# Kernel optimization log

Hardware: AMD Instinct MI355X
Metric: run time of the kernel (lower is better)

Reference implementation:

```python
import jax, jax.numpy as jnp
import numpy as np

N, M, H, K, CIN, COUT, P = 50000, 50000, 32, 15, 64, 128, 3
KP_EXTENT = 0.072
RADIUS = 0.06


def setup_inputs() -> dict:
    key = jax.random.key(0)
    ks = jax.random.split(key, 7)
    q_pts = jax.random.uniform(ks[0], (N, P), dtype=jnp.float32) * 0.05
    s_pts = jax.random.uniform(ks[1], (M, P), dtype=jnp.float32) * 0.05
    neighb_inds = jax.random.randint(ks[2], (N, H), 0, M, dtype=jnp.int64)
    x = jax.random.normal(ks[3], (M, CIN), dtype=jnp.float32)
    # kernel points inside sphere of radius RADIUS (stand-in for load_kernels)
    kernel_points = jax.random.normal(ks[4], (K, P), dtype=jnp.float32) * (0.5 * RADIUS)
    stddev = np.sqrt(1.0 / (K * COUT)).astype(np.float32)
    weights = jax.random.normal(ks[5], (K, CIN, COUT), dtype=jnp.float32) * stddev
    bias = jnp.zeros((COUT,), dtype=jnp.float32)
    return {"q_pts": q_pts, "s_pts": s_pts, "neighb_inds": neighb_inds,
            "x": x, "kernel_points": kernel_points, "weights": weights, "bias": bias}


def reference(q_pts, s_pts, neighb_inds, x, kernel_points, weights, bias):
    # pad support points with a far-away point and features with a zero row
    s_pad = jnp.concatenate([s_pts, jnp.full((1, s_pts.shape[1]), 1e6, s_pts.dtype)], axis=0)
    x_pad = jnp.concatenate([x, jnp.zeros((1, x.shape[1]), x.dtype)], axis=0)
    # gather neighbor coords/features: [N, H, P], [N, H, CIN]
    neighbors = s_pad[neighb_inds] - q_pts[:, None, :]
    neighb_x = x_pad[neighb_inds]
    # distances to kernel points: [N, H, K]
    diff = neighbors[:, :, None, :] - kernel_points  # [N, H, K, P]
    sq_d = jnp.sum(diff * diff, axis=-1)
    all_weights = jax.nn.relu(1.0 - jnp.sqrt(sq_d) / KP_EXTENT)  # linear influence
    # aggregate: [N, K, CIN] then apply per-kernel-point weights and sum over K
    weighted_features = jnp.einsum('nhk,nhc->nkc', all_weights, neighb_x)
    out = jnp.einsum('nkc,kco->no', weighted_features, weights) + bias  # [N, COUT]
    return out
```

## Files before the change

kernel.cpp:

```cpp
#include <hip/hip_runtime.h>
#include <hip/hip_bf16.h>


#define NPTS   50000
#define NPAD   50048
#define HNB    32
#define KPTS   15
#define CING   64
#define COUTG  128
#define KDIM   960
#define INV_EXT 13.888889f

typedef __attribute__((ext_vector_type(8))) short bf16x8;
typedef __attribute__((ext_vector_type(4))) float f32x4;

static __device__ __forceinline__ unsigned short f2bf(float f) {
    unsigned int u = __float_as_uint(f);
    u += 0x7FFFu + ((u >> 16) & 1u);
    return (unsigned short)(u >> 16);
}

__global__ void kpconv_wt(const float* __restrict__ wgt, unsigned short* __restrict__ Wt) {
    int kc = blockIdx.x;
    int o  = threadIdx.x;
    Wt[(size_t)o * KDIM + kc] = f2bf(wgt[(size_t)kc * COUTG + o]);
}

__global__ __launch_bounds__(256) void kpconv_agg(
    const float* __restrict__ q_pts, const float* __restrict__ s_pts,
    const int* __restrict__ inds, const float* __restrict__ x,
    const float* __restrict__ kpts, unsigned short* __restrict__ wf)
{
    __shared__ float kp[48];
    __shared__ float nb[4][HNB][3];
    __shared__ int   sidx[4][HNB];
    __shared__ float w[4][HNB][16];

    const int tid = threadIdx.x;
    const int g   = tid >> 6;
    const int c   = tid & 63;
    const int n   = blockIdx.x * 4 + g;

    if (tid < 45) kp[tid] = kpts[tid];
    if (c < HNB) {
        int m = inds[n * HNB + c];
        sidx[g][c] = m;
        float qx = q_pts[n * 3 + 0];
        float qy = q_pts[n * 3 + 1];
        float qz = q_pts[n * 3 + 2];
        nb[g][c][0] = s_pts[(size_t)m * 3 + 0] - qx;
        nb[g][c][1] = s_pts[(size_t)m * 3 + 1] - qy;
        nb[g][c][2] = s_pts[(size_t)m * 3 + 2] - qz;
    }
    __syncthreads();

    for (int i = c; i < 512; i += 64) {
        int h = i >> 4, k = i & 15;
        float v = 0.f;
        if (k < KPTS) {
            float dx = nb[g][h][0] - kp[k * 3 + 0];
            float dy = nb[g][h][1] - kp[k * 3 + 1];
            float dz = nb[g][h][2] - kp[k * 3 + 2];
            float d  = sqrtf(dx * dx + dy * dy + dz * dz);
            v = fmaxf(0.f, 1.f - d * INV_EXT);
        }
        w[g][h][k] = v;
    }
    __syncthreads();

    float acc[KPTS];
#pragma unroll
    for (int k = 0; k < KPTS; ++k) acc[k] = 0.f;

#pragma unroll 8
    for (int h = 0; h < HNB; ++h) {
        float xv = x[(size_t)sidx[g][h] * CING + c];
        float4 w0 = *(float4*)&w[g][h][0];
        float4 w1 = *(float4*)&w[g][h][4];
        float4 w2 = *(float4*)&w[g][h][8];
        float4 w3 = *(float4*)&w[g][h][12];
        acc[0]  = fmaf(w0.x, xv, acc[0]);
        acc[1]  = fmaf(w0.y, xv, acc[1]);
        acc[2]  = fmaf(w0.z, xv, acc[2]);
        acc[3]  = fmaf(w0.w, xv, acc[3]);
        acc[4]  = fmaf(w1.x, xv, acc[4]);
        acc[5]  = fmaf(w1.y, xv, acc[5]);
        acc[6]  = fmaf(w1.z, xv, acc[6]);
        acc[7]  = fmaf(w1.w, xv, acc[7]);
        acc[8]  = fmaf(w2.x, xv, acc[8]);
        acc[9]  = fmaf(w2.y, xv, acc[9]);
        acc[10] = fmaf(w2.z, xv, acc[10]);
        acc[11] = fmaf(w2.w, xv, acc[11]);
        acc[12] = fmaf(w3.x, xv, acc[12]);
        acc[13] = fmaf(w3.y, xv, acc[13]);
        acc[14] = fmaf(w3.z, xv, acc[14]);
    }

#pragma unroll
    for (int k = 0; k < KPTS; ++k)
        wf[(size_t)n * KDIM + k * CING + c] = f2bf(acc[k]);
}

#define BK    32
#define LDP   40

__global__ __launch_bounds__(256) void kpconv_gemm(
    const unsigned short* __restrict__ A,
    const unsigned short* __restrict__ Bt,
    const float* __restrict__ bias,
    float* __restrict__ out)
{
    __shared__ unsigned short As[128 * LDP];
    __shared__ unsigned short Bs[128 * LDP];

    const int tid  = threadIdx.x;
    const int wave = tid >> 6;
    const int lane = tid & 63;
    const int l15  = lane & 15;
    const int quad = lane >> 4;
    const long blockM = (long)blockIdx.x * 128;

    f32x4 acc[2][8];
#pragma unroll
    for (int i = 0; i < 2; ++i)
#pragma unroll
        for (int j = 0; j < 8; ++j) acc[i][j] = (f32x4){0.f, 0.f, 0.f, 0.f};

    const int srow = tid >> 1;
    const int scol = (tid & 1) * 16;
    const size_t aBase = (size_t)(blockM + srow) * KDIM + scol;
    const size_t bBase = (size_t)srow * KDIM + scol;

    for (int kk = 0; kk < KDIM; kk += BK) {
        uint4 a0 = *(const uint4*)(A + aBase + kk);
        uint4 a1 = *(const uint4*)(A + aBase + kk + 8);
        uint4 b0 = *(const uint4*)(Bt + bBase + kk);
        uint4 b1 = *(const uint4*)(Bt + bBase + kk + 8);
        __syncthreads();
        *(uint4*)&As[srow * LDP + scol]     = a0;
        *(uint4*)&As[srow * LDP + scol + 8] = a1;
        *(uint4*)&Bs[srow * LDP + scol]     = b0;
        *(uint4*)&Bs[srow * LDP + scol + 8] = b1;
        __syncthreads();

        bf16x8 af[2], bfr[8];
#pragma unroll
        for (int mf = 0; mf < 2; ++mf)
            af[mf] = *(bf16x8*)&As[(wave * 32 + mf * 16 + l15) * LDP + quad * 8];
#pragma unroll
        for (int nf = 0; nf < 8; ++nf)
            bfr[nf] = *(bf16x8*)&Bs[(nf * 16 + l15) * LDP + quad * 8];
#pragma unroll
        for (int mf = 0; mf < 2; ++mf)
#pragma unroll
            for (int nf = 0; nf < 8; ++nf)
                acc[mf][nf] = __builtin_amdgcn_mfma_f32_16x16x32_bf16(
                    af[mf], bfr[nf], acc[mf][nf], 0, 0, 0);
    }

#pragma unroll
    for (int mf = 0; mf < 2; ++mf) {
        long r0 = blockM + wave * 32 + mf * 16 + quad * 4;
#pragma unroll
        for (int nf = 0; nf < 8; ++nf) {
            int col = nf * 16 + l15;
            float bv = bias[col];
#pragma unroll
            for (int r = 0; r < 4; ++r) {
                long row = r0 + r;
                if (row < NPTS) out[row * COUTG + col] = acc[mf][nf][r] + bv;
            }
        }
    }
}

extern "C" void kernel_launch(void* const* d_in, const int* in_sizes, int n_in,
                              void* d_out, int out_size, void* d_ws, size_t ws_size,
                              hipStream_t stream) {
    const float* q_pts = (const float*)d_in[0];
    const float* s_pts = (const float*)d_in[1];
    const int*   inds  = (const int*)d_in[2];
    const float* x     = (const float*)d_in[3];
    const float* kpts  = (const float*)d_in[4];
    const float* wgt   = (const float*)d_in[5];
    const float* bias  = (const float*)d_in[6];
    float* out = (float*)d_out;

    unsigned short* wf = (unsigned short*)d_ws;
    unsigned short* Wt = wf + (size_t)NPAD * KDIM;

    kpconv_wt<<<KDIM, COUTG, 0, stream>>>(wgt, Wt);
    kpconv_agg<<<NPTS / 4, 256, 0, stream>>>(q_pts, s_pts, inds, x, kpts, wf);
    kpconv_gemm<<<NPAD / 128, 256, 0, stream>>>(wf, Wt, bias, out);
}
```

Measured before the change: 193.1 us.

## Use MFMA for neighbor aggregation with bf16 features and retile GEMM with prefetch

Adds a pre-pass that converts the input features x to bf16. The aggregation kernel now computes the per-point influence weights straight into MFMA fragments and runs the weighted neighbor sum as bf16 MFMAs, which drops the shared-memory weight table and the scalar FMA loop. The GEMM now uses 64-row tiles with a 64-wide K step and register prefetch of the next tile to raise occupancy and hide load latency. The feature gather now reads 2-byte elements, one per lane, which may coalesce poorly, and the weighted sum loses precision because its inputs are bf16.

After: 159.5 us. 17.4% less time.

```diff
diff --git a/kernel.cpp b/kernel.cpp
--- a/kernel.cpp
+++ b/kernel.cpp
@@ -9,9 +9,11 @@
 #define CING   64
 #define COUTG  128
 #define KDIM   960
+#define MSUP   50000
 #define INV_EXT 13.888889f
 
 typedef __attribute__((ext_vector_type(8))) short bf16x8;
+typedef __attribute__((ext_vector_type(8))) unsigned short u16x8;
 typedef __attribute__((ext_vector_type(4))) float f32x4;
 
 static __device__ __forceinline__ unsigned short f2bf(float f) {
@@ -20,156 +22,169 @@
     return (unsigned short)(u >> 16);
 }
 
+__global__ __launch_bounds__(256) void kpconv_x2bf(const float* __restrict__ x,
+                                                   unsigned short* __restrict__ xb) {
+    int i = (blockIdx.x * 256 + threadIdx.x) * 8;
+    if (i >= MSUP * CING) return;
+    float4 a = *(const float4*)(x + i);
+    float4 b = *(const float4*)(x + i + 4);
+    u16x8 o;
+    o[0] = f2bf(a.x); o[1] = f2bf(a.y); o[2] = f2bf(a.z); o[3] = f2bf(a.w);
+    o[4] = f2bf(b.x); o[5] = f2bf(b.y); o[6] = f2bf(b.z); o[7] = f2bf(b.w);
+    *(u16x8*)(xb + i) = o;
+}
+
 __global__ void kpconv_wt(const float* __restrict__ wgt, unsigned short* __restrict__ Wt) {
     int kc = blockIdx.x;
     int o  = threadIdx.x;
     Wt[(size_t)o * KDIM + kc] = f2bf(wgt[(size_t)kc * COUTG + o]);
 }
 
-__global__ __launch_bounds__(256) void kpconv_agg(
+__global__ __launch_bounds__(256) void kpconv_agg2(
     const float* __restrict__ q_pts, const float* __restrict__ s_pts,
-    const int* __restrict__ inds, const float* __restrict__ x,
+    const int* __restrict__ inds, const unsigned short* __restrict__ xb,
     const float* __restrict__ kpts, unsigned short* __restrict__ wf)
 {
-    __shared__ float kp[48];
-    __shared__ float nb[4][HNB][3];
-    __shared__ int   sidx[4][HNB];
-    __shared__ float w[4][HNB][16];
-
-    const int tid = threadIdx.x;
-    const int g   = tid >> 6;
-    const int c   = tid & 63;
-    const int n   = blockIdx.x * 4 + g;
-
-    if (tid < 45) kp[tid] = kpts[tid];
-    if (c < HNB) {
-        int m = inds[n * HNB + c];
-        sidx[g][c] = m;
+    __shared__ float4 nb4[4][HNB];
+
+    const int tid  = threadIdx.x;
+    const int g    = tid >> 6;
+    const int lane = tid & 63;
+    const int l15  = lane & 15;
+    const int quad = lane >> 4;
+    const int n    = blockIdx.x * 4 + g;
+
+    if (lane < HNB) {
+        int m = inds[n * HNB + lane];
         float qx = q_pts[n * 3 + 0];
         float qy = q_pts[n * 3 + 1];
         float qz = q_pts[n * 3 + 2];
-        nb[g][c][0] = s_pts[(size_t)m * 3 + 0] - qx;
-        nb[g][c][1] = s_pts[(size_t)m * 3 + 1] - qy;
-        nb[g][c][2] = s_pts[(size_t)m * 3 + 2] - qz;
+        nb4[g][lane] = make_float4(s_pts[m * 3 + 0] - qx,
+                                   s_pts[m * 3 + 1] - qy,
+                                   s_pts[m * 3 + 2] - qz,
+                                   __int_as_float(m));
     }
     __syncthreads();
 
-    for (int i = c; i < 512; i += 64) {
-        int h = i >> 4, k = i & 15;
-        float v = 0.f;
-        if (k < KPTS) {
-            float dx = nb[g][h][0] - kp[k * 3 + 0];
-            float dy = nb[g][h][1] - kp[k * 3 + 1];
-            float dz = nb[g][h][2] - kp[k * 3 + 2];
-            float d  = sqrtf(dx * dx + dy * dy + dz * dz);
-            v = fmaxf(0.f, 1.f - d * INV_EXT);
-        }
-        w[g][h][k] = v;
-    }
-    __syncthreads();
-
-    float acc[KPTS];
-#pragma unroll
-    for (int k = 0; k < KPTS; ++k) acc[k] = 0.f;
-
-#pragma unroll 8
-    for (int h = 0; h < HNB; ++h) {
-        float xv = x[(size_t)sidx[g][h] * CING + c];
-        float4 w0 = *(float4*)&w[g][h][0];
-        float4 w1 = *(float4*)&w[g][h][4];
-        float4 w2 = *(float4*)&w[g][h][8];
-        float4 w3 = *(float4*)&w[g][h][12];
-        acc[0]  = fmaf(w0.x, xv, acc[0]);
-        acc[1]  = fmaf(w0.y, xv, acc[1]);
-        acc[2]  = fmaf(w0.z, xv, acc[2]);
-        acc[3]  = fmaf(w0.w, xv, acc[3]);
-        acc[4]  = fmaf(w1.x, xv, acc[4]);
-        acc[5]  = fmaf(w1.y, xv, acc[5]);
-        acc[6]  = fmaf(w1.z, xv, acc[6]);
-        acc[7]  = fmaf(w1.w, xv, acc[7]);
-        acc[8]  = fmaf(w2.x, xv, acc[8]);
-        acc[9]  = fmaf(w2.y, xv, acc[9]);
-        acc[10] = fmaf(w2.z, xv, acc[10]);
-        acc[11] = fmaf(w2.w, xv, acc[11]);
-        acc[12] = fmaf(w3.x, xv, acc[12]);
-        acc[13] = fmaf(w3.y, xv, acc[13]);
-        acc[14] = fmaf(w3.z, xv, acc[14]);
-    }
-
-#pragma unroll
-    for (int k = 0; k < KPTS; ++k)
-        wf[(size_t)n * KDIM + k * CING + c] = f2bf(acc[k]);
-}
-
-#define BK    32
-#define LDP   40
-
-__global__ __launch_bounds__(256) void kpconv_gemm(
+    const bool kvalid = (l15 < KPTS);
+    const int  kidx   = kvalid ? l15 : 0;
+    const float kx = kpts[kidx * 3 + 0];
+    const float ky = kpts[kidx * 3 + 1];
+    const float kz = kpts[kidx * 3 + 2];
+
+    bf16x8 af;
+    int mrow[8];
+#pragma unroll
+    for (int j = 0; j < 8; ++j) {
+        float4 v = nb4[g][quad * 8 + j];
+        mrow[j] = __float_as_int(v.w);
+        float dx = v.x - kx, dy = v.y - ky, dz = v.z - kz;
+        float d  = sqrtf(dx * dx + dy * dy + dz * dz);
+        float w  = kvalid ? fmaxf(0.f, 1.f - d * INV_EXT) : 0.f;
+        af[j] = (short)f2bf(w);
+    }
+
+    f32x4 acc[4];
+#pragma unroll
+    for (int nt = 0; nt < 4; ++nt) acc[nt] = (f32x4){0.f, 0.f, 0.f, 0.f};
+
+#pragma unroll
+    for (int nt = 0; nt < 4; ++nt) {
+        const int c = nt * 16 + l15;
+        bf16x8 bfr;
+#pragma unroll
+        for (int j = 0; j < 8; ++j)
+            bfr[j] = (short)xb[((size_t)mrow[j] << 6) + c];
+        acc[nt] = __builtin_amdgcn_mfma_f32_16x16x32_bf16(af, bfr, acc[nt], 0, 0, 0);
+    }
+
+    const size_t base = (size_t)n * KDIM;
+#pragma unroll
+    for (int nt = 0; nt < 4; ++nt) {
+        const int c = nt * 16 + l15;
+#pragma unroll
+        for (int r = 0; r < 4; ++r) {
+            int k = quad * 4 + r;
+            if (k < KPTS) wf[base + k * CING + c] = f2bf(acc[nt][r]);
+        }
+    }
+}
+
+#define GBM 64
+#define GBK 64
+#define GLP 72
+
+__global__ __launch_bounds__(256) void kpconv_gemm2(
     const unsigned short* __restrict__ A,
     const unsigned short* __restrict__ Bt,
     const float* __restrict__ bias,
     float* __restrict__ out)
 {
-    __shared__ unsigned short As[128 * LDP];
-    __shared__ unsigned short Bs[128 * LDP];
+    __shared__ unsigned short As[GBM * GLP];
+    __shared__ unsigned short Bs[COUTG * GLP];
 
     const int tid  = threadIdx.x;
     const int wave = tid >> 6;
     const int lane = tid & 63;
     const int l15  = lane & 15;
     const int quad = lane >> 4;
-    const long blockM = (long)blockIdx.x * 128;
-
-    f32x4 acc[2][8];
-#pragma unroll
-    for (int i = 0; i < 2; ++i)
-#pragma unroll
-        for (int j = 0; j < 8; ++j) acc[i][j] = (f32x4){0.f, 0.f, 0.f, 0.f};
-
-    const int srow = tid >> 1;
-    const int scol = (tid & 1) * 16;
-    const size_t aBase = (size_t)(blockM + srow) * KDIM + scol;
-    const size_t bBase = (size_t)srow * KDIM + scol;
-
-    for (int kk = 0; kk < KDIM; kk += BK) {
-        uint4 a0 = *(const uint4*)(A + aBase + kk);
-        uint4 a1 = *(const uint4*)(A + aBase + kk + 8);
-        uint4 b0 = *(const uint4*)(Bt + bBase + kk);
-        uint4 b1 = *(const uint4*)(Bt + bBase + kk + 8);
+    const long blockM = (long)blockIdx.x * GBM;
+
+    f32x4 acc[8];
+#pragma unroll
+    for (int i = 0; i < 8; ++i) acc[i] = (f32x4){0.f, 0.f, 0.f, 0.f};
+
+    const int arow = tid >> 2, acol = (tid & 3) * 16;
+    const int brow = tid >> 1, bcol = (tid & 1) * 32;
+    const unsigned short* aptr = A + (size_t)(blockM + arow) * KDIM + acol;
+    const unsigned short* bptr = Bt + (size_t)brow * KDIM + bcol;
+
+    uint4 ra0 = *(const uint4*)(aptr);
+    uint4 ra1 = *(const uint4*)(aptr + 8);
+    uint4 rb0 = *(const uint4*)(bptr);
+    uint4 rb1 = *(const uint4*)(bptr + 8);
+    uint4 rb2 = *(const uint4*)(bptr + 16);
+    uint4 rb3 = *(const uint4*)(bptr + 24);
+
+    for (int kk = 0; kk < KDIM; kk += GBK) {
         __syncthreads();
-        *(uint4*)&As[srow * LDP + scol]     = a0;
-        *(uint4*)&As[srow * LDP + scol + 8] = a1;
-        *(uint4*)&Bs[srow * LDP + scol]     = b0;
-        *(uint4*)&Bs[srow * LDP + scol + 8] = b1;
+        *(uint4*)&As[arow * GLP + acol]      = ra0;
+        *(uint4*)&As[arow * GLP + acol + 8]  = ra1;
+        *(uint4*)&Bs[brow * GLP + bcol]      = rb0;
+        *(uint4*)&Bs[brow * GLP + bcol + 8]  = rb1;
+        *(uint4*)&Bs[brow * GLP + bcol + 16] = rb2;
+        *(uint4*)&Bs[brow * GLP + bcol + 24] = rb3;
         __syncthreads();
 
-        bf16x8 af[2], bfr[8];
-#pragma unroll
-        for (int mf = 0; mf < 2; ++mf)
-            af[mf] = *(bf16x8*)&As[(wave * 32 + mf * 16 + l15) * LDP + quad * 8];
-#pragma unroll
-        for (int nf = 0; nf < 8; ++nf)
-            bfr[nf] = *(bf16x8*)&Bs[(nf * 16 + l15) * LDP + quad * 8];
-#pragma unroll
-        for (int mf = 0; mf < 2; ++mf)
-#pragma unroll
-            for (int nf = 0; nf < 8; ++nf)
-                acc[mf][nf] = __builtin_amdgcn_mfma_f32_16x16x32_bf16(
-                    af[mf], bfr[nf], acc[mf][nf], 0, 0, 0);
-    }
-
-#pragma unroll
-    for (int mf = 0; mf < 2; ++mf) {
-        long r0 = blockM + wave * 32 + mf * 16 + quad * 4;
-#pragma unroll
-        for (int nf = 0; nf < 8; ++nf) {
-            int col = nf * 16 + l15;
-            float bv = bias[col];
-#pragma unroll
-            for (int r = 0; r < 4; ++r) {
-                long row = r0 + r;
-                if (row < NPTS) out[row * COUTG + col] = acc[mf][nf][r] + bv;
+        if (kk + GBK < KDIM) {
+            ra0 = *(const uint4*)(aptr + kk + GBK);
+            ra1 = *(const uint4*)(aptr + kk + GBK + 8);
+            rb0 = *(const uint4*)(bptr + kk + GBK);
+            rb1 = *(const uint4*)(bptr + kk + GBK + 8);
+            rb2 = *(const uint4*)(bptr + kk + GBK + 16);
+            rb3 = *(const uint4*)(bptr + kk + GBK + 24);
+        }
+
+#pragma unroll
+        for (int ch = 0; ch < 2; ++ch) {
+            bf16x8 afr = *(bf16x8*)&As[(wave * 16 + l15) * GLP + ch * 32 + quad * 8];
+#pragma unroll
+            for (int nf = 0; nf < 8; ++nf) {
+                bf16x8 bfr = *(bf16x8*)&Bs[(nf * 16 + l15) * GLP + ch * 32 + quad * 8];
+                acc[nf] = __builtin_amdgcn_mfma_f32_16x16x32_bf16(afr, bfr, acc[nf], 0, 0, 0);
             }
+        }
+    }
+
+    const long r0 = blockM + wave * 16 + quad * 4;
+#pragma unroll
+    for (int nf = 0; nf < 8; ++nf) {
+        const int col = nf * 16 + l15;
+        const float bv = bias[col];
+#pragma unroll
+        for (int r = 0; r < 4; ++r) {
+            long row = r0 + r;
+            if (row < NPTS) out[row * COUTG + col] = acc[nf][r] + bv;
         }
     }
 }
@@ -187,9 +202,11 @@
     float* out = (float*)d_out;
 
     unsigned short* wf = (unsigned short*)d_ws;
-    unsigned short* Wt = wf + (size_t)NPAD * KDIM;
-
+    unsigned short* xb = wf + (size_t)NPAD * KDIM;
+    unsigned short* Wt = xb + (size_t)MSUP * CING;
+
+    kpconv_x2bf<<<(MSUP * CING / 8 + 255) / 256, 256, 0, stream>>>(x, xb);
     kpconv_wt<<<KDIM, COUTG, 0, stream>>>(wgt, Wt);
-    kpconv_agg<<<NPTS / 4, 256, 0, stream>>>(q_pts, s_pts, inds, x, kpts, wf);
-    kpconv_gemm<<<NPAD / 128, 256, 0, stream>>>(wf, Wt, bias, out);
-}
+    kpconv_agg2<<<NPTS / 4, 256, 0, stream>>>(q_pts, s_pts, inds, xb, kpts, wf);
+    kpconv_gemm2<<<NPAD / GBM, 256, 0, stream>>>(wf, Wt, bias, out);
+}
```
